# Kernel optimization log

Measured on AMD Instinct MI355X. Metric: run time of the kernel, lower is better.

Reference implementation:

```python
import jax, jax.numpy as jnp
import numpy as np

BATCH = 4
N_PER = 300          # queries per image (equal split -> cum_feats_batch = [0,300,600,900,1200])
NUM_FEATS = BATCH * N_PER
IN_DIM = 256
KEY_DIM = 32
FH = FW = 160


def setup_inputs() -> dict:
    key = jax.random.key(0)
    ks = jax.random.split(key, 6)
    return {
        "in_feats": jax.random.normal(ks[0], (NUM_FEATS, IN_DIM), dtype=jnp.float32),
        "feat_map": jax.random.normal(ks[1], (BATCH, IN_DIM, FH, FW), dtype=jnp.float32),
        "qry_w": jax.random.normal(ks[2], (KEY_DIM, IN_DIM), dtype=jnp.float32) * 0.05,
        "qry_b": jax.random.normal(ks[3], (KEY_DIM,), dtype=jnp.float32) * 0.05,
        "key_w": jax.random.normal(ks[4], (KEY_DIM, IN_DIM), dtype=jnp.float32) * 0.05,
        "key_b": jax.random.normal(ks[5], (KEY_DIM,), dtype=jnp.float32) * 0.05,
    }


def reference(in_feats, feat_map, qry_w, qry_b, key_w, key_b):
    # qry module: Linear projecting input features -> dynamic conv weights  [NF, C]
    qry_feats = in_feats @ qry_w.T + qry_b
    # key module: 1x1 conv on the first feature map  [B, C, H, W]
    key_map = jnp.einsum('oc,bchw->bohw', key_w, feat_map) + key_b[None, :, None, None]
    # per-batch dynamic 1x1 conv: F.conv2d(key_map[i:i+1], qry_feats[i0:i1,:,None,None])
    # with an equal split of queries per image this is a batched einsum.
    q = qry_feats.reshape(BATCH, N_PER, KEY_DIM)            # [B, N, C]
    seg_logits = jnp.einsum('bnc,bchw->bnhw', q, key_map)   # [B, N, H, W]
    return seg_logits.reshape(NUM_FEATS, FH, FW)            # [num_feats, fH, fW]
```

## Files before the change

kernel.cpp:

```cpp
#include <hip/hip_runtime.h>
#include <hip/hip_bf16.h>

#define BATCH 4
#define N_PER 300
#define IN_DIM 256
#define KEY_DIM 32
#define FH 160
#define FW 160
#define HW (FH * FW)
#define NQ (BATCH * N_PER)
#define Q_ELEMS (NQ * KEY_DIM)
#define KWT_ELEMS (IN_DIM * KEY_DIM)
#define PREP_TOTAL (Q_ELEMS + KWT_ELEMS)

__global__ __launch_bounds__(256) void prep_kernel(
        const float* __restrict__ in_feats,
        const float* __restrict__ qry_w,
        const float* __restrict__ qry_b,
        const float* __restrict__ key_w,
        float* __restrict__ ws) {
    int gid = blockIdx.x * 256 + threadIdx.x;
    if (gid < Q_ELEMS) {
        int n = gid >> 5;
        int c = gid & 31;
        const float* __restrict__ fr = in_feats + n * IN_DIM;
        const float* __restrict__ wr = qry_w + c * IN_DIM;
        float a0 = qry_b[c], a1 = 0.f, a2 = 0.f, a3 = 0.f;
        #pragma unroll 4
        for (int k = 0; k < IN_DIM; k += 4) {
            a0 += fr[k + 0] * wr[k + 0];
            a1 += fr[k + 1] * wr[k + 1];
            a2 += fr[k + 2] * wr[k + 2];
            a3 += fr[k + 3] * wr[k + 3];
        }
        ws[gid] = (a0 + a1) + (a2 + a3);
    } else {
        int i = gid - Q_ELEMS;
        int c = i >> 5;
        int o = i & 31;
        ws[gid] = key_w[o * IN_DIM + c];
    }
}

__global__ __launch_bounds__(256) void main_kernel(
        const float* __restrict__ feat_map,
        const float* __restrict__ key_b,
        const float* __restrict__ ws,
        float* __restrict__ out) {
    const int b = blockIdx.y;
    const int p = blockIdx.x * 256 + threadIdx.x;

    const float* __restrict__ fb  = feat_map + ((size_t)b * IN_DIM) * HW + p;
    const float* __restrict__ kwT = ws + Q_ELEMS;

    float key[KEY_DIM];
    #pragma unroll
    for (int o = 0; o < KEY_DIM; ++o) key[o] = key_b[o];

    #pragma unroll 8
    for (int c = 0; c < IN_DIM; ++c) {
        float f = fb[(size_t)c * HW];
        const float* __restrict__ kr = kwT + c * KEY_DIM;
        #pragma unroll
        for (int o = 0; o < KEY_DIM; ++o)
            key[o] += kr[o] * f;
    }

    const float* __restrict__ qb = ws + (size_t)b * N_PER * KEY_DIM;
    float* __restrict__ ob = out + ((size_t)b * N_PER) * HW + p;
    for (int n = 0; n < N_PER; ++n) {
        const float* __restrict__ qn = qb + n * KEY_DIM;
        float a0 = 0.f, a1 = 0.f, a2 = 0.f, a3 = 0.f;
        #pragma unroll
        for (int c = 0; c < KEY_DIM; c += 4) {
            a0 += qn[c + 0] * key[c + 0];
            a1 += qn[c + 1] * key[c + 1];
            a2 += qn[c + 2] * key[c + 2];
            a3 += qn[c + 3] * key[c + 3];
        }
        ob[(size_t)n * HW] = (a0 + a1) + (a2 + a3);
    }
}

extern "C" void kernel_launch(void* const* d_in, const int* in_sizes, int n_in,
                              void* d_out, int out_size, void* d_ws, size_t ws_size,
                              hipStream_t stream) {
    const float* in_feats = (const float*)d_in[0];
    const float* feat_map = (const float*)d_in[1];
    const float* qry_w    = (const float*)d_in[2];
    const float* qry_b    = (const float*)d_in[3];
    const float* key_w    = (const float*)d_in[4];
    const float* key_b    = (const float*)d_in[5];
    float* ws  = (float*)d_ws;
    float* out = (float*)d_out;

    prep_kernel<<<dim3(PREP_TOTAL / 256), dim3(256), 0, stream>>>(
        in_feats, qry_w, qry_b, key_w, ws);

    dim3 grid(HW / 256, BATCH);
    main_kernel<<<grid, dim3(256), 0, stream>>>(feat_map, key_b, ws, out);
}
```

Before: 281.0 us.

## Split main kernel into keymap and chunked seg kernels for more parallelism

The fused main kernel is split in two. The first computes the 32-dim key map per pixel and writes it to workspace. The second reads it back and computes logits over query chunks along a third grid dimension, which gives four times as many blocks to fill the GPU during the output-write-bound phase. The prep kernel also stages the transposed qry_w in shared memory and loads in_feats with float4. In exchange there is an extra key-map round trip through global memory and one more launch.

```diff
diff --git a/kernel.cpp b/kernel.cpp
--- a/kernel.cpp
+++ b/kernel.cpp
@@ -1,5 +1,4 @@
 #include <hip/hip_runtime.h>
-#include <hip/hip_bf16.h>
 
 #define BATCH 4
 #define N_PER 300
@@ -12,6 +11,10 @@
 #define Q_ELEMS (NQ * KEY_DIM)
 #define KWT_ELEMS (IN_DIM * KEY_DIM)
 #define PREP_TOTAL (Q_ELEMS + KWT_ELEMS)
+#define KM_OFF PREP_TOTAL
+#define KM_ELEMS (BATCH * HW * KEY_DIM)
+#define NCH 75
+#define NCHUNKS (N_PER / NCH)
 
 __global__ __launch_bounds__(256) void prep_kernel(
         const float* __restrict__ in_feats,
@@ -19,19 +22,37 @@
         const float* __restrict__ qry_b,
         const float* __restrict__ key_w,
         float* __restrict__ ws) {
-    int gid = blockIdx.x * 256 + threadIdx.x;
+    __shared__ float qw[IN_DIM * 33];
+    const int t = threadIdx.x;
+    {
+        int o = t >> 3;
+        int kbase = (t & 7) * 32;
+        const float4* __restrict__ src = (const float4*)(qry_w + o * IN_DIM + kbase);
+        #pragma unroll
+        for (int j = 0; j < 32; j += 4) {
+            float4 v = src[j >> 2];
+            qw[(kbase + j + 0) * 33 + o] = v.x;
+            qw[(kbase + j + 1) * 33 + o] = v.y;
+            qw[(kbase + j + 2) * 33 + o] = v.z;
+            qw[(kbase + j + 3) * 33 + o] = v.w;
+        }
+    }
+    __syncthreads();
+
+    int gid = blockIdx.x * 256 + t;
     if (gid < Q_ELEMS) {
         int n = gid >> 5;
         int c = gid & 31;
-        const float* __restrict__ fr = in_feats + n * IN_DIM;
-        const float* __restrict__ wr = qry_w + c * IN_DIM;
+        const float4* __restrict__ fr4 = (const float4*)(in_feats + n * IN_DIM);
         float a0 = qry_b[c], a1 = 0.f, a2 = 0.f, a3 = 0.f;
         #pragma unroll 4
-        for (int k = 0; k < IN_DIM; k += 4) {
-            a0 += fr[k + 0] * wr[k + 0];
-            a1 += fr[k + 1] * wr[k + 1];
-            a2 += fr[k + 2] * wr[k + 2];
-            a3 += fr[k + 3] * wr[k + 3];
+        for (int k4 = 0; k4 < IN_DIM / 4; ++k4) {
+            float4 f = fr4[k4];
+            int k = k4 * 4;
+            a0 += f.x * qw[(k + 0) * 33 + c];
+            a1 += f.y * qw[(k + 1) * 33 + c];
+            a2 += f.z * qw[(k + 2) * 33 + c];
+            a3 += f.w * qw[(k + 3) * 33 + c];
         }
         ws[gid] = (a0 + a1) + (a2 + a3);
     } else {
@@ -42,22 +63,21 @@
     }
 }
 
-__global__ __launch_bounds__(256) void main_kernel(
+__global__ __launch_bounds__(256) void keymap_kernel(
         const float* __restrict__ feat_map,
         const float* __restrict__ key_b,
-        const float* __restrict__ ws,
-        float* __restrict__ out) {
+        float* __restrict__ ws) {
     const int b = blockIdx.y;
     const int p = blockIdx.x * 256 + threadIdx.x;
 
-    const float* __restrict__ fb  = feat_map + ((size_t)b * IN_DIM) * HW + p;
+    const float* __restrict__ fb  = feat_map + (size_t)b * IN_DIM * HW + p;
     const float* __restrict__ kwT = ws + Q_ELEMS;
 
     float key[KEY_DIM];
     #pragma unroll
     for (int o = 0; o < KEY_DIM; ++o) key[o] = key_b[o];
 
-    #pragma unroll 8
+    #pragma unroll 16
     for (int c = 0; c < IN_DIM; ++c) {
         float f = fb[(size_t)c * HW];
         const float* __restrict__ kr = kwT + c * KEY_DIM;
@@ -66,9 +86,31 @@
             key[o] += kr[o] * f;
     }
 
-    const float* __restrict__ qb = ws + (size_t)b * N_PER * KEY_DIM;
-    float* __restrict__ ob = out + ((size_t)b * N_PER) * HW + p;
-    for (int n = 0; n < N_PER; ++n) {
+    float* __restrict__ kmp = ws + KM_OFF + ((size_t)(b * HW) + p) * KEY_DIM;
+    #pragma unroll
+    for (int o = 0; o < KEY_DIM; o += 4)
+        *(float4*)(kmp + o) = make_float4(key[o], key[o + 1], key[o + 2], key[o + 3]);
+}
+
+__global__ __launch_bounds__(256) void seg_kernel(
+        const float* __restrict__ ws,
+        float* __restrict__ out) {
+    const int b  = blockIdx.y;
+    const int p  = blockIdx.x * 256 + threadIdx.x;
+    const int n0 = blockIdx.z * NCH;
+
+    const float* __restrict__ kmp = ws + KM_OFF + ((size_t)(b * HW) + p) * KEY_DIM;
+    float key[KEY_DIM];
+    #pragma unroll
+    for (int o = 0; o < KEY_DIM; o += 4) {
+        float4 v = *(const float4*)(kmp + o);
+        key[o] = v.x; key[o + 1] = v.y; key[o + 2] = v.z; key[o + 3] = v.w;
+    }
+
+    const float* __restrict__ qb = ws + ((size_t)b * N_PER + n0) * KEY_DIM;
+    float* __restrict__ ob = out + ((size_t)(b * N_PER + n0)) * HW + p;
+    #pragma unroll 3
+    for (int n = 0; n < NCH; ++n) {
         const float* __restrict__ qn = qb + n * KEY_DIM;
         float a0 = 0.f, a1 = 0.f, a2 = 0.f, a3 = 0.f;
         #pragma unroll
@@ -97,6 +139,8 @@
     prep_kernel<<<dim3(PREP_TOTAL / 256), dim3(256), 0, stream>>>(
         in_feats, qry_w, qry_b, key_w, ws);
 
-    dim3 grid(HW / 256, BATCH);
-    main_kernel<<<grid, dim3(256), 0, stream>>>(feat_map, key_b, ws, out);
+    keymap_kernel<<<dim3(HW / 256, BATCH), dim3(256), 0, stream>>>(
+        feat_map, key_b, ws);
+
+    seg_kernel<<<dim3(HW / 256, BATCH, NCHUNKS), dim3(256), 0, stream>>>(ws, out);
 }
```

Result: slower. 304.2 us (+8.2%).
